# Kernel tuning notes

Hardware: AMD Instinct MI355X
Metric: run time of the kernel (lower is better)

## Reference

```python
import jax, jax.numpy as jnp
import numpy as np
from math import lgamma

# Architecture constants hardcoded in the original S2ConvNet
B_IN, B1, B2 = 30, 10, 6
F1, F2, F_OUT = 20, 40, 10
C64 = jnp.complex64


def _lf(n):
    return np.array([lgamma(i + 1.0) for i in range(n + 1)])


def _wigner_d(L, betas):
    """Padded Wigner-d tensor [L, nbeta, 2L-1, 2L-1]; entry [l,:,m+L-1,n+L-1] = d^l_{mn}(beta),
    zero where |m|>l or |n|>l. Explicit Wigner formula with log-factorials (stable for l<=30)."""
    nb = len(betas)
    out = np.zeros((L, nb, 2 * L - 1, 2 * L - 1))
    cb, sb = np.cos(betas / 2.0), np.sin(betas / 2.0)
    lf = _lf(4 * L)
    for l in range(L):
        for m in range(-l, l + 1):
            for n in range(-l, l + 1):
                pref = 0.5 * (lf[l + m] + lf[l - m] + lf[l + n] + lf[l - n])
                acc = np.zeros(nb)
                for s in range(max(0, n - m), min(l + n, l - m) + 1):
                    c = pref - (lf[l + n - s] + lf[s] + lf[m - n + s] + lf[l - m - s])
                    acc += (-1.0) ** (m - n + s) * np.exp(c) * cb ** (2 * l + n - m - 2 * s) * sb ** (m - n + 2 * s)
                out[l, :, m + L - 1, n + L - 1] = acc
    return out


def _dh_beta(b):
    return np.pi * (2 * np.arange(2 * b) + 1) / (4.0 * b)


def _dh_w(b):
    # Driscoll-Healy quadrature weights over the beta ring
    beta = _dh_beta(b)
    j = np.arange(b)
    return (2.0 / b) * np.sin(beta) * np.sum(np.sin((2 * j[:, None] + 1) * beta[None, :]) / (2 * j[:, None] + 1), axis=0)


def _s2_grid(max_beta=np.pi / 8, n_alpha=8, n_beta=3):
    beta = (np.arange(n_beta) + 1) * max_beta / n_beta
    alpha = np.linspace(0, 2 * np.pi, n_alpha, endpoint=False)
    B, A = np.meshgrid(beta, alpha, indexing='ij')
    return B.ravel(), A.ravel()


def _so3_grid(max_beta=np.pi / 8, n_alpha=8, n_beta=3, n_gamma=6):
    beta = (np.arange(n_beta) + 1) * max_beta / n_beta
    alpha = np.linspace(0, 2 * np.pi, n_alpha, endpoint=False)
    gamma = np.linspace(0, 2 * np.pi, n_gamma, endpoint=False)
    B, A, G = np.meshgrid(beta, alpha, gamma, indexing='ij')
    return B.ravel(), A.ravel(), G.ravel()


# ---- precomputed spectral constants (trace-time numpy) ----
_m1 = np.arange(-(B1 - 1), B1)            # 19 retained azimuthal freqs for b_l1
_m2 = np.arange(-(B2 - 1), B2)            # 11 retained freqs for b_l2
_mi_in = _m1 % (2 * B_IN)                 # wrap into fft bins of size 60
_mi_b1 = _m1 % (2 * B1)                   # wrap into bins of size 20
_mi2_b1 = _m2 % (2 * B1)
_mi2_b2 = _m2 % (2 * B2)

# S2 FFT: quadrature-weighted d^l_{m,0}(beta_k) on the b_in beta grid  [10,60,19]
_wd_s2 = (_dh_w(B_IN)[None, :, None] * _wigner_d(B1, _dh_beta(B_IN))[:, :, :, B1 - 1]).astype(np.float32)
# S2 kernel rft basis: conj spherical harmonics at the 24 near-identity grid pts  [10,24,19]
_bg, _ag = _s2_grid()
_Y1 = (_wigner_d(B1, _bg)[:, :, :, B1 - 1] * np.exp(-1j * _m1[None, :] * _ag[:, None])[None]).astype(np.complex64)
# SO3 inverse FFT synthesis matrices (incl. (2l+1) plancherel weight)  [10,20,19,19]
_d1w = (_wigner_d(B1, _dh_beta(B1)) * (2 * np.arange(B1) + 1)[:, None, None, None]).astype(np.float32)
# SO3 forward FFT analysis matrices (quadrature-weighted)  [6,20,11,11]
_d12w = (_wigner_d(B2, _dh_beta(B1)) * _dh_w(B1)[None, :, None, None]).astype(np.float32)
# SO3 kernel rft basis: conj Wigner-D at the 144 grid pts  [6,144,11,11]
_bg2, _ag2, _gg2 = _so3_grid()
_D2 = (_wigner_d(B2, _bg2) * np.exp(-1j * (_m2[None, :, None] * _ag2[:, None, None] + _m2[None, None, :] * _gg2[:, None, None]))[None]).astype(np.complex64)
_d2w = (_wigner_d(B2, _dh_beta(B2)) * (2 * np.arange(B2) + 1)[:, None, None, None]).astype(np.float32)
_w2n = (_dh_w(B2) / _dh_w(B2).sum()).astype(np.float32)


def _forward(x, psi1, psi2, w_lin, b_lin):
    B = x.shape[0]
    # ---- S2Convolution: azimuthal FFT + Legendre transform -> spectral outer product -> SO3 iFFT
    xf = jnp.fft.fft(x, axis=-1)[..., _mi_in]                       # [B,1,60,19] (beta, m)
    X = jnp.einsum('lbm,zcbm->lzcm', jnp.asarray(_wd_s2), xf)        # [10,B,1,19]
    Psi1 = jnp.einsum('iog,lgm->liom', psi1.astype(C64), jnp.asarray(_Y1))  # [10,1,20,19]
    F = jnp.einsum('lzcm,lcon->lzomn', X, Psi1)                      # [10,B,20,19,19]
    Fh = jnp.einsum('lzomn,lbmn->zobmn', F, jnp.asarray(_d1w))       # [B,20,20beta,19,19]
    full = jnp.zeros((B, F1, 2 * B1, 2 * B1, 2 * B1), C64).at[..., _mi_b1[:, None], _mi_b1[None, :]].set(Fh)
    y = jax.nn.relu(jnp.fft.ifft2(full, axes=(-2, -1)).real * (2 * B1) ** 2)  # [B,20,20,20,20] (beta,alpha,gamma)

    # ---- SO3Convolution: SO3 FFT -> per-l batched complex matmul -> SO3 iFFT
    yf = jnp.fft.fftn(y, axes=(-2, -1))[..., _mi2_b1[:, None], _mi2_b1[None, :]]  # [B,20,20,11,11]
    Fx = jnp.einsum('lbmn,zcbmn->lzcmn', jnp.asarray(_d12w), yf)     # [6,B,20,11,11]
    Psi2 = jnp.einsum('iog,lgmn->liomn', psi2.astype(C64), jnp.asarray(_D2))      # [6,20,40,11,11]
    Fo = jnp.einsum('lzimk,liokn->lzomn', Fx, Psi2)                  # [6,B,40,11,11]
    Fh2 = jnp.einsum('lzomn,lbmn->zobmn', Fo, jnp.asarray(_d2w))     # [B,40,12beta,11,11]
    full2 = jnp.zeros((B, F2, 2 * B2, 2 * B2, 2 * B2), C64).at[..., _mi2_b2[:, None], _mi2_b2[None, :]].set(Fh2)
    y2 = jax.nn.relu(jnp.fft.ifft2(full2, axes=(-2, -1)).real * (2 * B2) ** 2)    # [B,40,12,12,12]

    # ---- so3_integrate (beta quadrature, uniform alpha/gamma) + linear head
    feat = jnp.einsum('zobag,b->zo', y2, jnp.asarray(_w2n)) / (2 * B2) ** 2       # [B,40]
    return feat @ w_lin.T + b_lin


def setup_inputs() -> dict:
    key = jax.random.key(0)
    k1, k2, k3, k4, k5 = jax.random.split(key, 5)
    return {
        'x': jax.random.normal(k1, (128, 1, 60, 60), jnp.float32),
        'psi1': jax.random.normal(k2, (1, 20, 24), jnp.float32) * 0.1,
        'psi2': jax.random.normal(k3, (20, 40, 144), jnp.float32) * 0.05,
        'w_lin': jax.random.normal(k4, (10, 40), jnp.float32) * 0.1,
        'b_lin': jax.random.normal(k5, (10,), jnp.float32) * 0.1,
    }


def reference(x, psi1, psi2, w_lin, b_lin):
    return _forward(x, psi1, psi2, w_lin, b_lin)
```

## Files before the change

kernel.cpp:

```cpp
#include <hip/hip_runtime.h>
#include <math.h>

#define PI_D 3.14159265358979323846
#define PI_F 3.14159265358979f

#define BATCH 128
#define NM1 19
#define NMP1 10
#define NM2 11
#define NMP2 6
#define NB_IN 60
#define NB1 20
#define NB2 12
#define NL1 10
#define NL2 6
#define F1C 20
#define F2C 40
#define NBC 5

#define GEMM_MH (BATCH*NMP2)
#define GEMM_N (F2C*NM2)
#define GEMM_K (F1C*NM2)
#define GM 64
#define GN 64
#define GK 20
#define ASTR 21

#define TW_SYNT 0
#define TW_SYNA 380
#define TW_ANAA 580
#define TW_ANAG 700
#define TW_S2   940
#define TW_60   1072
#define TW_TOT  1672

#define TTS 22

#define N_D1WC 40000
#define N_D12WC 7920
#define N_WIGY 570
#define N_WIGD2 2178
#define N_D2W  (NL2*NB2*NM2*NM2)
#define N_WDS2C 6000
#define N_W2N  (NB2)
#define N_CSMALL (N_WIGY+N_WIGD2+N_WDS2C+N_W2N)
#define N_CPREP (N_D1WC+N_D12WC+N_D2W)
#define PREP_BASE (BATCH + 1 + 120)
#define NBLK_CPREP ((N_CPREP + 255)/256)

__device__ __forceinline__ float ipow_f(float x, int e) {
  float r = 1.f;
  for (int i = 0; i < e; ++i) r *= x;
  return r;
}

__device__ float wigdf(const float* lf, int l, int m, int n, float beta) {
  if (m < -l || m > l || n < -l || n > l) return 0.f;
  float cb = cosf(0.5f*beta), sb = sinf(0.5f*beta);
  float pref = 0.5f*(lf[l+m]+lf[l-m]+lf[l+n]+lf[l-n]);
  int s0 = (n-m) > 0 ? (n-m) : 0;
  int s1 = (l+n) < (l-m) ? (l+n) : (l-m);
  float acc = 0.f;
  for (int s = s0; s <= s1; ++s) {
    float lc = pref - (lf[l+n-s]+lf[s]+lf[m-n+s]+lf[l-m-s]);
    float tt = expf(lc) * ipow_f(cb, 2*l+n-m-2*s) * ipow_f(sb, m-n+2*s);
    acc += ((m-n+s) & 1) ? -tt : tt;
  }
  return acc;
}

__device__ __forceinline__ float dh_beta_f(int b, int k) {
  return (float)(PI_D*(2*k+1)/(4.0*b));
}

__device__ float dh_w_f(int b, int k) {
  float beta = dh_beta_f(b, k), s = 0.f;
  for (int j = 0; j < b; ++j) s += sinf((2.f*(float)j+1.f)*beta)/(2.f*(float)j+1.f);
  return (2.f/(float)b)*sinf(beta)*s;
}

__global__ __launch_bounds__(256) void k_consts1(float2* __restrict__ Tg,
                         float* __restrict__ wigY, float* __restrict__ wigD2,
                         float* __restrict__ wd_s2c, float* __restrict__ w2n) {
  __shared__ float lf[41];
  __shared__ float dhw30[60], dhw6[12];
  int t = threadIdx.x;
  if (t < 41) lf[t] = (float)lgamma((double)t + 1.0);
  else if (t < 101) dhw30[t-41] = dh_w_f(30, t-41);
  else if (t < 113) dhw6[t-101] = dh_w_f(6, t-101);
  __syncthreads();

  if (blockIdx.x == 0) {
    for (int i = t; i < TW_TOT; i += 256) {
      float2 v;
      if (i < TW_SYNA) {
        int j = i, n = j/NB1, g = j%NB1;
        int r = (g*(n-9)) % NB1; if (r < 0) r += NB1;
        float s, c; sincosf(2.f*PI_F*(float)r/(float)NB1, &s, &c);
        v = make_float2(c, s);
      } else if (i < TW_ANAA) {
        int j = i - TW_SYNA, a = j/NMP1, mp = j%NMP1;
        int r = (a*mp) % NB1;
        float s, c; sincosf(2.f*PI_F*(float)r/(float)NB1, &s, &c);
        v = make_float2(c, s);
      } else if (i < TW_ANAG) {
        int j = i - TW_ANAA, a = j/NMP2, m2p = j%NMP2;
        int r = (a*m2p) % NB1;
        float s, c; sincosf(2.f*PI_F*(float)r/(float)NB1, &s, &c);
        v = make_float2(c, -s);
      } else if (i < TW_S2) {
        int j = i - TW_ANAG, g = j/12, cI = j%12;
        if (cI == 11) v = make_float2(0.f, 0.f);
        else {
          int r = (g*(cI-5)) % NB1; if (r < 0) r += NB1;
          float s, c; sincosf(2.f*PI_F*(float)r/(float)NB1, &s, &c);
          v = make_float2(c, -s);
        }
      } else if (i < TW_60) {
        int j = i - TW_S2, k = j/NM2, mi = j%NM2;
        int r = (k*(mi-5)) % NB2; if (r < 0) r += NB2;
        float s, c; sincosf(2.f*PI_F*(float)r/(float)NB2, &s, &c);
        v = make_float2(c, s);
      } else {
        int j = i - TW_60, a = j/NMP1, mp = j%NMP1;
        int r = (a*mp) % NB_IN;
        float s, c; sincosf(2.f*PI_F*(float)r/(float)NB_IN, &s, &c);
        v = make_float2(c, -s);
      }
      Tg[i] = v;
    }
  }

  int gid = blockIdx.x*blockDim.x + t;

  if (gid < N_WIGY) {
    int l = gid/57; int r = gid%57; int bidx = r/19; int mi = r%19;
    float beta = (float)((double)(bidx + 1) * PI_D/24.0);
    wigY[gid] = wigdf(lf, l, mi-9, 0, beta);
    return;
  }
  gid -= N_WIGY;
  if (gid < N_WIGD2) {
    int l = gid/363; int r = gid%363; int bidx = r/121; int mn = r%121;
    int m = mn/NM2 - 5, n = mn%NM2 - 5;
    float beta = (float)((double)(bidx + 1) * PI_D/24.0);
    wigD2[gid] = wigdf(lf, l, m, n, beta);
    return;
  }
  gid -= N_WIGD2;
  if (gid < N_WDS2C) {
    int l = gid/600; int r = gid%600; int k = r/10; int mp = r%10;
    wd_s2c[gid] = dhw30[k] * wigdf(lf, l, mp, 0, dh_beta_f(30,k));
    return;
  }
  gid -= N_WDS2C;
  if (gid < N_W2N) {
    float s = 0.f;
    for (int j = 0; j < NB2; ++j) s += dhw6[j];
    w2n[gid] = dhw6[gid]/s;
    return;
  }
}

#define P2IO 40
#define P2GC 24
__global__ __launch_bounds__(256) void k_prep(const float* __restrict__ x,
                                              const float* __restrict__ wd_s2c,
                                              const float2* __restrict__ Tg,
                                              const float* __restrict__ wigY,
                                              const float* __restrict__ wigD2,
                                              const float* __restrict__ psi1,
                                              const float* __restrict__ psi2,
                                              float2* __restrict__ X,
                                              float2* __restrict__ Psi1p,
                                              float2* __restrict__ Bm,
                                              float* __restrict__ d1wc,
                                              float* __restrict__ d12wc,
                                              float* __restrict__ d2w) {
  __shared__ __align__(16) float smem[6912];
  const int bid = blockIdx.x, t = threadIdx.x;

  if (bid < BATCH) {
    const int z = bid;
    float*  xs   = smem;
    float2* xf   = (float2*)(smem + 3600);
    float2* tw60 = (float2*)(smem + 4800);
    for (int i = t; i < NB_IN*NMP1; i += 256) tw60[i] = Tg[TW_60 + i];
    for (int i = t; i < 3600; i += 256) xs[i] = x[z*3600 + i];
    __syncthreads();
    for (int i = t; i < NB_IN*NMP1; i += 256) {
      int k = i/NMP1, mp = i%NMP1;
      float re = 0.f, im = 0.f;
      const float* xrow = &xs[k*NB_IN];
      for (int a = 0; a < NB_IN; ++a) {
        float v = xrow[a];
        float2 e = tw60[a*NMP1 + mp];
        re = fmaf(v, e.x, re);
        im = fmaf(v, e.y, im);
      }
      xf[i] = make_float2(re, im);
    }
    __syncthreads();
    for (int i = t; i < NL1*NMP1; i += 256) {
      int l = i/NMP1, mp = i%NMP1;
      float re = 0.f, im = 0.f;
      for (int k = 0; k < NB_IN; ++k) {
        float w = wd_s2c[(l*NB_IN+k)*NMP1 + mp];
        float2 v = xf[k*NMP1 + mp];
        re = fmaf(w, v.x, re); im = fmaf(w, v.y, im);
      }
      X[(l*BATCH + z)*NMP1 + mp] = make_float2(re, im);
    }
    return;
  }

  if (bid == BATCH) {
    float*  wigYs = smem;
    float*  psis  = smem + 576;
    float2* ph8   = (float2*)(smem + 1056);
    for (int i = t; i < N_WIGY; i += 256) wigYs[i] = wigY[i];
    for (int i = t; i < F1C*24; i += 256) psis[i] = psi1[i];
    if (t < 8) {
      float s, c; sincosf(2.f*PI_F*(float)t/8.f, &s, &c);
      ph8[t] = make_float2(c, s);
    }
    __syncthreads();
    for (int i = t; i < NL1*F1C*NM1; i += 256) {
      int l = i/(F1C*NM1); int r = i%(F1C*NM1); int o = r/NM1; int mi = r%NM1;
      int m = mi - 9;
      float re = 0.f, im = 0.f;
      for (int g = 0; g < 24; ++g) {
        float w = psis[o*24 + g];
        float d = wigYs[(l*3 + (g >> 3))*NM1 + mi];
        int pa = g & 7;
        int rr = (-(m*pa)) % 8; if (rr < 0) rr += 8;
        float2 ph = ph8[rr];
        re = fmaf(w, d*ph.x, re); im = fmaf(w, d*ph.y, im);
      }
      Psi1p[i] = make_float2(re, im);
    }
    return;
  }

  if (bid < PREP_BASE) {
    const int j = bid - (BATCH + 1);
    const int io0 = (j/NL2)*P2IO, l = j%NL2;
    float2* Ds   = (float2*)smem;
    float*  Ws   = smem + 5856;
    float2* ph24 = (float2*)(smem + 6816);
    const int tio = t/31, tmn = t%31;
    const int mn0 = tmn*4;
    if (t < 24) {
      float s, c; sincosf(2.f*PI_F*(float)t/24.f, &s, &c);
      ph24[t] = make_float2(c, s);
    }
    __syncthreads();
    float2 acc[5][4];
    #pragma unroll
    for (int i = 0; i < 5; ++i)
      #pragma unroll
      for (int jj = 0; jj < 4; ++jj) acc[i][jj] = make_float2(0.f, 0.f);

    for (int gc = 0; gc < 144; gc += P2GC) {
      for (int i = t; i < P2GC*121; i += 256) {
        int g = i/121, mn = i%121;
        int p = gc + g;
        int m = mn/NM2 - 5, n = mn%NM2 - 5;
        float d = wigD2[(l*3 + p/48)*121 + mn];
        int pa = (p/6)%8, pg = p%6;
        int rr24 = (-(3*m*pa + 4*n*pg)) % 24; if (rr24 < 0) rr24 += 24;
        float2 ph = ph24[rr24];
        Ds[g*122 + mn] = make_float2(d*ph.x, d*ph.y);
      }
      for (int i = t; i < P2IO*P2GC; i += 256) {
        int io = i/P2GC, g = i%P2GC;
        Ws[i] = psi2[(io0 + io)*144 + gc + g];
      }
      __syncthreads();
      if (tio < 8) {
        for (int g = 0; g < P2GC; ++g) {
          float4 d01 = *(const float4*)&Ds[g*122 + mn0];
          float4 d23 = *(const float4*)&Ds[g*122 + mn0 + 2];
          float w0 = Ws[(tio*5 + 0)*P2GC + g];
          float w1 = Ws[(tio*5 + 1)*P2GC + g];
          float w2 = Ws[(tio*5 + 2)*P2GC + g];
          float w3 = Ws[(tio*5 + 3)*P2GC + g];
          float w4 = Ws[(tio*5 + 4)*P2GC + g];
          float dx[4] = {d01.x, d01.z, d23.x, d23.z};
          float dy[4] = {d01.y, d01.w, d23.y, d23.w};
          float wv[5] = {w0, w1, w2, w3, w4};
          #pragma unroll
          for (int i = 0; i < 5; ++i)
            #pragma unroll
            for (int jj = 0; jj < 4; ++jj) {
              acc[i][jj].x = fmaf(wv[i], dx[jj], acc[i][jj].x);
              acc[i][jj].y = fmaf(wv[i], dy[jj], acc[i][jj].y);
            }
        }
      }
      __syncthreads();
    }
    if (tio < 8) {
      #pragma unroll
      for (int i = 0; i < 5; ++i) {
        int io = io0 + tio*5 + i;
        int ii = io/F2C, oo = io%F2C;
        #pragma unroll
        for (int jj = 0; jj < 4; ++jj) {
          int mn = mn0 + jj;
          if (mn < 121) {
            int k = mn/NM2, n = mn%NM2;
            Bm[(size_t)l*GEMM_K*GEMM_N + (ii*NM2 + k)*GEMM_N + oo*NM2 + n] = acc[i][jj];
          }
        }
      }
    }
    return;
  }

  {
    float* lf     = smem;
    float* dhw10l = smem + 48;
    if (t < 41) lf[t] = (float)lgamma((double)t + 1.0);
    else if (t >= 64 && t < 84) dhw10l[t-64] = dh_w_f(10, t-64);
    __syncthreads();
    int idx = (bid - PREP_BASE)*256 + t;
    if (idx < N_D1WC) {
      int l = idx/4000; int r = idx%4000; int b = r/200; int r2 = r%200;
      int mp = r2/20, nn = r2%20;
      d1wc[idx] = (nn < NM1) ? (float)(2*l+1) * wigdf(lf, l, mp, nn-9, dh_beta_f(10,b)) : 0.f;
      return;
    }
    idx -= N_D1WC;
    if (idx < N_D12WC) {
      int l2 = idx/1320; int r = idx%1320; int b = r/66; int r2 = r%66;
      int m2p = r2/11, n2i = r2%11;
      d12wc[idx] = dhw10l[b] * wigdf(lf, l2, m2p, n2i-5, dh_beta_f(10,b));
      return;
    }
    idx -= N_D12WC;
    if (idx < N_D2W) {
      int l = idx/(NB2*NM2*NM2); int r = idx%(NB2*NM2*NM2); int j = r/(NM2*NM2); int rr = r%(NM2*NM2);
      int m = rr/NM2 - 5, n = rr%NM2 - 5;
      d2w[idx] = (float)(2*l+1) * wigdf(lf, l, m, n, dh_beta_f(6,j));
      return;
    }
  }
}

__global__ __launch_bounds__(256) void k_stage1(const float2* __restrict__ X,
                                                const float2* __restrict__ Psi1,
                                                const float* __restrict__ d1wc,
                                                const float* __restrict__ d12wc,
                                                const float2* __restrict__ Tg,
                                                float2* __restrict__ Am) {
  __shared__ float2 Xs[NL1*NMP1];
  __shared__ float2 Ps[NL1*NM1];
  __shared__ __align__(16) float2 XPp[NL1*NMP1*20];
  __shared__ __align__(16) float2 Etab[978];
  __shared__ __align__(16) float2 bufA[NBC*200];
  __shared__ __align__(16) float2 bufB[NBC*220];
  __shared__ float2 yfs[NBC*NMP2*NM2];
  __shared__ float2 Fxa[NL2*NMP2*NM2];

  const int z = blockIdx.x, o = blockIdx.y, t = threadIdx.x;
  const float2* EsynTp = Etab;
  const float2* EsynA  = Etab + 418;
  const float2* EanaA  = Etab + 618;
  const float2* EanaG  = Etab + 738;

  for (int i = t; i < 978; i += 256) {
    float2 v;
    if (i < 418) {
      int n = i/TTS, g = i%TTS;
      v = (g < NB1) ? Tg[TW_SYNT + n*NB1 + g] : make_float2(0.f, 0.f);
    } else {
      v = Tg[TW_SYNA + (i - 418)];
    }
    Etab[i] = v;
  }
  for (int i = t; i < NL1*NMP1; i += 256) {
    int l = i/NMP1, mp = i%NMP1;
    Xs[i] = X[(l*BATCH + z)*NMP1 + mp];
  }
  for (int i = t; i < NL1*NM1; i += 256) {
    int l = i/NM1, mi = i%NM1;
    Ps[i] = Psi1[(l*F1C + o)*NM1 + mi];
  }
  for (int i = t; i < NL2*NMP2*NM2; i += 256) Fxa[i] = make_float2(0.f, 0.f);
  __syncthreads();

  for (int i = t; i < NL1*NMP1*20; i += 256) {
    int n = i % 20; int r = i/20; int mp = r % NMP1; int l = r/NMP1;
    float2 v = make_float2(0.f, 0.f);
    if (n < NM1) {
      float2 xa = Xs[l*NMP1+mp], pp = Ps[l*NM1+n];
      v = make_float2(xa.x*pp.x - xa.y*pp.y, xa.x*pp.y + xa.y*pp.x);
    }
    XPp[i] = v;
  }
  __syncthreads();

  float2* Fh = bufA;
  float2* Tt = bufB;
  float*  yb = (float*)bufA;
  float2* Uu = bufB;

  for (int c = 0; c < NB1/NBC; ++c) {
    const int b0 = c*NBC;
    for (int i = t; i < NBC*NMP1*5; i += 256) {
      int q = i % 5; int r = i/5; int mp = r % NMP1; int bb = r/NMP1;
      int n0 = q*4;
      const float* dw = &d1wc[((b0+bb)*NMP1 + mp)*20 + n0];
      const float2* xp = &XPp[mp*20 + n0];
      float2 a0 = {0.f,0.f}, a1 = {0.f,0.f}, a2 = {0.f,0.f}, a3 = {0.f,0.f};
      #pragma unroll
      for (int l = 0; l < NL1; ++l) {
        float4 w4 = *(const float4*)&dw[l*4000];
        float4 xa = *(const float4*)&xp[l*(NMP1*20)];
        float4 xb = *(const float4*)&xp[l*(NMP1*20) + 2];
        a0.x = fmaf(w4.x, xa.x, a0.x); a0.y = fmaf(w4.x, xa.y, a0.y);
        a1.x = fmaf(w4.y, xa.z, a1.x); a1.y = fmaf(w4.y, xa.w, a1.y);
        a2.x = fmaf(w4.z, xb.x, a2.x); a2.y = fmaf(w4.z, xb.y, a2.y);
        a3.x = fmaf(w4.w, xb.z, a3.x); a3.y = fmaf(w4.w, xb.w, a3.y);
      }
      float2* fr = &Fh[(bb*NMP1 + mp)*NM1 + n0];
      fr[0] = a0; fr[1] = a1; fr[2] = a2;
      if (n0 + 3 < NM1) fr[3] = a3;
    }
    __syncthreads();
    for (int i = t; i < NBC*NMP1*5; i += 256) {
      int gq = i % 5; int r = i / 5; int mp = r % NMP1; int bb = r / NMP1;
      int g0 = gq*4;
      const float2* fh = &Fh[(bb*NMP1 + mp)*NM1];
      float2 a0 = {0.f,0.f}, a1 = {0.f,0.f}, a2 = {0.f,0.f}, a3 = {0.f,0.f};
      #pragma unroll
      for (int n = 0; n < NM1; ++n) {
        float2 f = fh[n];
        float4 e01 = *(const float4*)&EsynTp[n*TTS + g0];
        float4 e23 = *(const float4*)&EsynTp[n*TTS + g0 + 2];
        a0.x += f.x*e01.x - f.y*e01.y; a0.y += f.x*e01.y + f.y*e01.x;
        a1.x += f.x*e01.z - f.y*e01.w; a1.y += f.x*e01.w + f.y*e01.z;
        a2.x += f.x*e23.x - f.y*e23.y; a2.y += f.x*e23.y + f.y*e23.x;
        a3.x += f.x*e23.z - f.y*e23.w; a3.y += f.x*e23.w + f.y*e23.z;
      }
      float2* tr = &Tt[(bb*NMP1 + mp)*TTS + g0];
      tr[0] = a0; tr[1] = a1; tr[2] = a2; tr[3] = a3;
    }
    __syncthreads();
    for (int i = t; i < NBC*10*5; i += 256) {
      int gq = i % 5; int r = i / 5; int ap = r % 10; int bb = r / 10;
      int a0 = ap*2, g0 = gq*4;
      float4 t01 = *(const float4*)&Tt[(bb*NMP1)*TTS + g0];
      float4 t23 = *(const float4*)&Tt[(bb*NMP1)*TTS + g0 + 2];
      float s00=0.f,s01=0.f,s02=0.f,s03=0.f, s10=0.f,s11=0.f,s12=0.f,s13=0.f;
      #pragma unroll
      for (int mp = 1; mp < NMP1; ++mp) {
        float4 u01 = *(const float4*)&Tt[(bb*NMP1 + mp)*TTS + g0];
        float4 u23 = *(const float4*)&Tt[(bb*NMP1 + mp)*TTS + g0 + 2];
        float2 e0 = EsynA[a0*NMP1 + mp];
        float2 e1 = EsynA[(a0+1)*NMP1 + mp];
        s00 += e0.x*u01.x - e0.y*u01.y;
        s01 += e0.x*u01.z - e0.y*u01.w;
        s02 += e0.x*u23.x - e0.y*u23.y;
        s03 += e0.x*u23.z - e0.y*u23.w;
        s10 += e1.x*u01.x - e1.y*u01.y;
        s11 += e1.x*u01.z - e1.y*u01.w;
        s12 += e1.x*u23.x - e1.y*u23.y;
        s13 += e1.x*u23.z - e1.y*u23.w;
      }
      float* y0 = &yb[(bb*NB1 + a0)*NB1 + g0];
      float* y1 = &yb[(bb*NB1 + a0 + 1)*NB1 + g0];
      y0[0]=fmaxf(fmaf(2.f,s00,t01.x),0.f); y0[1]=fmaxf(fmaf(2.f,s01,t01.z),0.f);
      y0[2]=fmaxf(fmaf(2.f,s02,t23.x),0.f); y0[3]=fmaxf(fmaf(2.f,s03,t23.z),0.f);
      y1[0]=fmaxf(fmaf(2.f,s10,t01.x),0.f); y1[1]=fmaxf(fmaf(2.f,s11,t01.z),0.f);
      y1[2]=fmaxf(fmaf(2.f,s12,t23.x),0.f); y1[3]=fmaxf(fmaf(2.f,s13,t23.z),0.f);
    }
    __syncthreads();
    for (int i = t; i < NBC*NMP2*5; i += 256) {
      int gq = i % 5; int r = i / 5; int m2p = r % NMP2; int bb = r / NMP2;
      int g0 = gq*4;
      float2 u0 = {0.f,0.f}, u1 = {0.f,0.f}, u2 = {0.f,0.f}, u3 = {0.f,0.f};
      #pragma unroll
      for (int aa = 0; aa < NB1; ++aa) {
        float4 y4 = *(const float4*)&yb[(bb*NB1 + aa)*NB1 + g0];
        float2 e = EanaA[aa*NMP2 + m2p];
        u0.x = fmaf(y4.x, e.x, u0.x); u0.y = fmaf(y4.x, e.y, u0.y);
        u1.x = fmaf(y4.y, e.x, u1.x); u1.y = fmaf(y4.y, e.y, u1.y);
        u2.x = fmaf(y4.z, e.x, u2.x); u2.y = fmaf(y4.z, e.y, u2.y);
        u3.x = fmaf(y4.w, e.x, u3.x); u3.y = fmaf(y4.w, e.y, u3.y);
      }
      float2* ur = &Uu[(bb*NMP2 + m2p)*TTS + g0];
      ur[0] = u0; ur[1] = u1; ur[2] = u2; ur[3] = u3;
    }
    __syncthreads();
    for (int i = t; i < NBC*NMP2*6; i += 256) {
      int p = i % 6; int r = i / 6; int m2p = r % NMP2; int bb = r / NMP2;
      int n0 = p*2;
      const float2* ur = &Uu[(bb*NMP2 + m2p)*TTS];
      float2 acc0 = {0.f,0.f}, acc1 = {0.f,0.f};
      #pragma unroll
      for (int g = 0; g < NB1; ++g) {
        float2 u = ur[g];
        float4 e = *(const float4*)&EanaG[g*12 + n0];
        acc0.x += u.x*e.x - u.y*e.y; acc0.y += u.x*e.y + u.y*e.x;
        acc1.x += u.x*e.z - u.y*e.w; acc1.y += u.x*e.w + u.y*e.z;
      }
      yfs[(bb*NMP2 + m2p)*NM2 + n0] = acc0;
      if (n0 + 1 < NM2) yfs[(bb*NMP2 + m2p)*NM2 + n0 + 1] = acc1;
    }
    __syncthreads();
    for (int i = t; i < NL2*NMP2*NM2; i += 256) {
      int l2 = i/(NMP2*NM2); int r = i%(NMP2*NM2);
      float2 acc = Fxa[i];
      #pragma unroll
      for (int bb = 0; bb < NBC; ++bb) {
        float w = d12wc[(l2*NB1 + b0 + bb)*66 + r];
        float2 v = yfs[bb*(NMP2*NM2) + r];
        acc.x = fmaf(w, v.x, acc.x); acc.y = fmaf(w, v.y, acc.y);
      }
      Fxa[i] = acc;
    }
    __syncthreads();
  }
  for (int i = t; i < NL2*NMP2*NM2; i += 256) {
    int l2 = i/(NMP2*NM2); int r = i%(NMP2*NM2);
    int mp = r/NM2, n = r%NM2;
    Am[(size_t)l2*GEMM_MH*GEMM_K + (z*NMP2 + mp)*GEMM_K + o*NM2 + n] = Fxa[i];
  }
}

__global__ __launch_bounds__(256) void k_so3mm(const float2* __restrict__ A,
                                               const float2* __restrict__ B,
                                               float2* __restrict__ C0,
                                               float2* __restrict__ C1) {
  __shared__ float2 As[GM*ASTR];
  __shared__ float2 Bs[GK*GN];
  const int lz = blockIdx.z;
  const int l = lz >> 1, half = lz & 1;
  const int kbeg = half ? 120 : 0, klim = half ? 220 : 120;
  const int row0 = blockIdx.x*GM, col0 = blockIdx.y*GN;
  const int t = threadIdx.x;
  const float2* Ag = A + (size_t)l*GEMM_MH*GEMM_K;
  const float2* Bg = B + (size_t)l*GEMM_K*GEMM_N;
  float2* Cg = (half ? C1 : C0) + (size_t)l*GEMM_MH*GEMM_N;
  const int tn = t & 15, tm = t >> 4;
  float2 acc[4][4];
  #pragma unroll
  for (int i = 0; i < 4; ++i)
    #pragma unroll
    for (int j = 0; j < 4; ++j) acc[i][j] = make_float2(0.f, 0.f);

  for (int k0 = kbeg; k0 < klim; k0 += GK) {
    for (int i = t; i < GM*GK; i += 256) {
      int r = i/GK, kk = i%GK;
      As[r*ASTR + kk] = Ag[(size_t)(row0 + r)*GEMM_K + k0 + kk];
    }
    for (int i = t; i < GK*GN; i += 256) {
      int kk = i/GN, cc = i%GN;
      int col = col0 + cc;
      float2 v = (col < GEMM_N) ? Bg[(size_t)(k0 + kk)*GEMM_N + col] : make_float2(0.f, 0.f);
      Bs[(kk*4 + (cc & 3))*16 + (cc >> 2)] = v;
    }
    __syncthreads();
    #pragma unroll
    for (int kk = 0; kk < GK; ++kk) {
      float2 a[4], b[4];
      #pragma unroll
      for (int i = 0; i < 4; ++i) a[i] = As[(tm*4 + i)*ASTR + kk];
      #pragma unroll
      for (int j = 0; j < 4; ++j) b[j] = Bs[(kk*4 + j)*16 + tn];
      #pragma unroll
      for (int i = 0; i < 4; ++i)
        #pragma unroll
        for (int j = 0; j < 4; ++j) {
          acc[i][j].x = fmaf(a[i].x, b[j].x, acc[i][j].x);
          acc[i][j].x = fmaf(-a[i].y, b[j].y, acc[i][j].x);
          acc[i][j].y = fmaf(a[i].x, b[j].y, acc[i][j].y);
          acc[i][j].y = fmaf(a[i].y, b[j].x, acc[i][j].y);
        }
    }
    __syncthreads();
  }
  #pragma unroll
  for (int i = 0; i < 4; ++i) {
    int r = row0 + tm*4 + i;
    int c0 = col0 + tn*4;
    if (c0 < GEMM_N) {
      float4 v0 = make_float4(acc[i][0].x, acc[i][0].y, acc[i][1].x, acc[i][1].y);
      float4 v1 = make_float4(acc[i][2].x, acc[i][2].y, acc[i][3].x, acc[i][3].y);
      *(float4*)&Cg[(size_t)r*GEMM_N + c0] = v0;
      *(float4*)&Cg[(size_t)r*GEMM_N + c0 + 2] = v1;
    }
  }
}

__global__ __launch_bounds__(256) void k_stage2(const float2* __restrict__ C0,
                                                const float2* __restrict__ C1,
                                                const float* __restrict__ d2w,
                                                const float* __restrict__ w2n,
                                                const float2* __restrict__ Tg,
                                                float* __restrict__ feat) {
  __shared__ float2 Fos[NL2*NM2*NM2];
  __shared__ float2 Fh2[NB2*NM2*NM2];
  __shared__ float2 T2[NB2*NB2*NM2];
  __shared__ float2 Esyn2[NB2*NM2];
  __shared__ float w2s[NB2];
  __shared__ float wred[4];
  const int z = blockIdx.x, o = blockIdx.y, t = threadIdx.x;
  for (int i = t; i < NB2*NM2; i += 256) Esyn2[i] = Tg[TW_S2 + i];
  if (t < NB2) w2s[t] = w2n[t];
  for (int i = t; i < NL2*NM2*NM2; i += 256) {
    int l = i/(NM2*NM2); int mn = i%(NM2*NM2);
    int m = mn/NM2, n = mn%NM2;
    float2 v;
    if (m >= 5) {
      size_t idx = (size_t)l*GEMM_MH*GEMM_N + (size_t)(z*NMP2 + m - 5)*GEMM_N + o*NM2 + n;
      float2 a = C0[idx], b2 = C1[idx];
      v = make_float2(a.x + b2.x, a.y + b2.y);
    } else {
      size_t idx = (size_t)l*GEMM_MH*GEMM_N + (size_t)(z*NMP2 + 5 - m)*GEMM_N + o*NM2 + (10 - n);
      float2 a = C0[idx], b2 = C1[idx];
      float s = ((m - n) & 1) ? -1.f : 1.f;
      v = make_float2(s*(a.x + b2.x), -s*(a.y + b2.y));
    }
    Fos[i] = v;
  }
  __syncthreads();
  for (int i = t; i < NB2*NM2*NM2; i += 256) {
    int b = i/(NM2*NM2); int mn = i%(NM2*NM2);
    float re = 0.f, im = 0.f;
    #pragma unroll
    for (int l = 0; l < NL2; ++l) {
      float w = d2w[(l*NB2 + b)*(NM2*NM2) + mn];
      float2 v = Fos[l*(NM2*NM2) + mn];
      re = fmaf(w, v.x, re); im = fmaf(w, v.y, im);
    }
    Fh2[i] = make_float2(re, im);
  }
  __syncthreads();
  for (int i = t; i < NB2*NB2*NM2; i += 256) {
    int ni = i % NM2; int r = i / NM2; int aa = r % NB2; int b = r / NB2;
    const float2* fh = &Fh2[b*(NM2*NM2) + ni];
    float re = 0.f, im = 0.f;
    #pragma unroll
    for (int mi = 0; mi < NM2; ++mi) {
      float2 f = fh[mi*NM2]; float2 e = Esyn2[aa*NM2+mi];
      re += e.x*f.x - e.y*f.y;
      im += e.x*f.y + e.y*f.x;
    }
    T2[i] = make_float2(re, im);
  }
  __syncthreads();
  float accT = 0.f;
  for (int i = t; i < NB2*NB2*NB2; i += 256) {
    int g = i % NB2; int r = i / NB2; int aa = r % NB2; int b = r / NB2;
    const float2* trow = &T2[(b*NB2 + aa)*NM2];
    float v = 0.f;
    #pragma unroll
    for (int ni = 0; ni < NM2; ++ni) {
      float2 tv = trow[ni]; float2 e = Esyn2[g*NM2+ni];
      v += e.x*tv.x - e.y*tv.y;
    }
    accT += w2s[b]*fmaxf(v, 0.f);
  }
  #pragma unroll
  for (int off = 32; off > 0; off >>= 1) accT += __shfl_down(accT, off);
  if ((t & 63) == 0) wred[t >> 6] = accT;
  __syncthreads();
  if (t == 0) feat[z*F2C + o] = (wred[0]+wred[1]+wred[2]+wred[3]) / (float)(NB2*NB2);
}

__global__ void k_head(const float* __restrict__ feat, const float* __restrict__ w_lin,
                       const float* __restrict__ b_lin, float* __restrict__ out) {
  int idx = blockIdx.x*blockDim.x + threadIdx.x;
  if (idx >= BATCH*10) return;
  int z = idx/10, f = idx%10;
  float acc = b_lin[f];
  for (int o = 0; o < F2C; ++o) acc = fmaf(feat[z*F2C + o], w_lin[f*F2C + o], acc);
  out[idx] = acc;
}

extern "C" void kernel_launch(void* const* d_in, const int* in_sizes, int n_in,
                              void* d_out, int out_size, void* d_ws, size_t ws_size,
                              hipStream_t stream) {
  const float* x     = (const float*)d_in[0];
  const float* psi1  = (const float*)d_in[1];
  const float* psi2  = (const float*)d_in[2];
  const float* w_lin = (const float*)d_in[3];
  const float* b_lin = (const float*)d_in[4];
  float* out = (float*)d_out;
  float* ws  = (float*)d_ws;

  size_t off = 0;
  auto alloc = [&](size_t nfloats) { size_t o = off; off += (nfloats + 15) & ~(size_t)15; return o; };
  float2* Tglob = (float2*)(ws + alloc(2*TW_TOT));
  float*  d1wc  = ws + alloc(N_D1WC);
  float*  d12wc = ws + alloc(N_D12WC);
  float*  wigY  = ws + alloc(N_WIGY);
  float*  wigD2 = ws + alloc(N_WIGD2);
  float*  d2w   = ws + alloc(N_D2W);
  float*  wd_s2c= ws + alloc(N_WDS2C);
  float*  w2n   = ws + alloc(N_W2N);
  float2* X     = (float2*)(ws + alloc(2*(size_t)NL1*BATCH*NMP1));
  float2* Psi1p = (float2*)(ws + alloc(2*(size_t)NL1*F1C*NM1));
  float2* Bmat  = (float2*)(ws + alloc(2*(size_t)NL2*GEMM_K*GEMM_N));
  float2* Amat  = (float2*)(ws + alloc(2*(size_t)NL2*GEMM_MH*GEMM_K));
  float2* Cmat0 = (float2*)(ws + alloc(2*(size_t)NL2*GEMM_MH*GEMM_N));
  float2* Cmat1 = (float2*)(ws + alloc(2*(size_t)NL2*GEMM_MH*GEMM_N));
  float*  featp = ws + alloc((size_t)BATCH*F2C);
  if (ws_size < off*sizeof(float)) return;

  k_consts1<<<(N_CSMALL + 255)/256, 256, 0, stream>>>(Tglob, wigY, wigD2, wd_s2c, w2n);
  k_prep<<<PREP_BASE + NBLK_CPREP, 256, 0, stream>>>(x, wd_s2c, Tglob, wigY, wigD2,
                                                     psi1, psi2, X, Psi1p, Bmat,
                                                     d1wc, d12wc, d2w);
  k_stage1<<<dim3(BATCH, F1C), 256, 0, stream>>>(X, Psi1p, d1wc, d12wc, Tglob, Amat);
  k_so3mm<<<dim3(GEMM_MH/GM, (GEMM_N + GN - 1)/GN, 2*NL2), 256, 0, stream>>>(Amat, Bmat, Cmat0, Cmat1);
  k_stage2<<<dim3(BATCH, F2C), 256, 0, stream>>>(Cmat0, Cmat1, d2w, w2n, Tglob, featp);
  k_head<<<(BATCH*10 + 255)/256, 256, 0, stream>>>(featp, w_lin, b_lin, out);
}
```

Baseline: 284.4 us.

## Widen stage1 blocks to 512 threads and split GEMM K four ways

Stage1 now runs 512 threads per block and handles 10 beta rings per chunk instead of 5. Each phase becomes a single guarded pass, which halves the chunk iterations and the barriers. The padded twiddle table is replaced by a direct copy, and Ps/Xs now alias bufA. The SO(3) GEMM splits K into four partial products written to four buffers, which stage2 sums, giving the GEMM more blocks to schedule at the cost of extra partial-buffer traffic and more shared memory per stage1 block.

Result: slower. 317.0 us (+11.5%).

```diff
diff --git a/kernel.cpp b/kernel.cpp
--- a/kernel.cpp
+++ b/kernel.cpp
@@ -16,7 +16,7 @@
 #define NL2 6
 #define F1C 20
 #define F2C 40
-#define NBC 5
+#define NBC 10
 
 #define GEMM_MH (BATCH*NMP2)
 #define GEMM_N (F2C*NM2)
@@ -33,8 +33,6 @@
 #define TW_S2   940
 #define TW_60   1072
 #define TW_TOT  1672
-
-#define TTS 22
 
 #define N_D1WC 40000
 #define N_D12WC 7920
@@ -348,49 +346,40 @@
   }
 }
 
-__global__ __launch_bounds__(256) void k_stage1(const float2* __restrict__ X,
+__global__ __launch_bounds__(512) void k_stage1(const float2* __restrict__ X,
                                                 const float2* __restrict__ Psi1,
                                                 const float* __restrict__ d1wc,
                                                 const float* __restrict__ d12wc,
                                                 const float2* __restrict__ Tg,
                                                 float2* __restrict__ Am) {
-  __shared__ float2 Xs[NL1*NMP1];
-  __shared__ float2 Ps[NL1*NM1];
   __shared__ __align__(16) float2 XPp[NL1*NMP1*20];
-  __shared__ __align__(16) float2 Etab[978];
-  __shared__ __align__(16) float2 bufA[NBC*200];
-  __shared__ __align__(16) float2 bufB[NBC*220];
+  __shared__ __align__(16) float2 Etab[940];
+  __shared__ __align__(16) float2 bufA[2000];
+  __shared__ __align__(16) float2 bufB[2000];
   __shared__ float2 yfs[NBC*NMP2*NM2];
   __shared__ float2 Fxa[NL2*NMP2*NM2];
 
   const int z = blockIdx.x, o = blockIdx.y, t = threadIdx.x;
-  const float2* EsynTp = Etab;
-  const float2* EsynA  = Etab + 418;
-  const float2* EanaA  = Etab + 618;
-  const float2* EanaG  = Etab + 738;
-
-  for (int i = t; i < 978; i += 256) {
-    float2 v;
-    if (i < 418) {
-      int n = i/TTS, g = i%TTS;
-      v = (g < NB1) ? Tg[TW_SYNT + n*NB1 + g] : make_float2(0.f, 0.f);
-    } else {
-      v = Tg[TW_SYNA + (i - 418)];
-    }
-    Etab[i] = v;
-  }
-  for (int i = t; i < NL1*NMP1; i += 256) {
+  const float2* EsynT = Etab;
+  const float2* EsynA = Etab + 380;
+  const float2* EanaA = Etab + 580;
+  const float2* EanaG = Etab + 700;
+  float2* Ps = bufA;
+  float2* Xs = bufA + 190;
+
+  for (int i = t; i < 940; i += 512) Etab[i] = Tg[i];
+  for (int i = t; i < NL1*NMP1; i += 512) {
     int l = i/NMP1, mp = i%NMP1;
     Xs[i] = X[(l*BATCH + z)*NMP1 + mp];
   }
-  for (int i = t; i < NL1*NM1; i += 256) {
+  for (int i = t; i < NL1*NM1; i += 512) {
     int l = i/NM1, mi = i%NM1;
     Ps[i] = Psi1[(l*F1C + o)*NM1 + mi];
   }
-  for (int i = t; i < NL2*NMP2*NM2; i += 256) Fxa[i] = make_float2(0.f, 0.f);
+  for (int i = t; i < NL2*NMP2*NM2; i += 512) Fxa[i] = make_float2(0.f, 0.f);
   __syncthreads();
 
-  for (int i = t; i < NL1*NMP1*20; i += 256) {
+  for (int i = t; i < NL1*NMP1*20; i += 512) {
     int n = i % 20; int r = i/20; int mp = r % NMP1; int l = r/NMP1;
     float2 v = make_float2(0.f, 0.f);
     if (n < NM1) {
@@ -408,8 +397,8 @@
 
   for (int c = 0; c < NB1/NBC; ++c) {
     const int b0 = c*NBC;
-    for (int i = t; i < NBC*NMP1*5; i += 256) {
-      int q = i % 5; int r = i/5; int mp = r % NMP1; int bb = r/NMP1;
+    if (t < 500) {
+      int q = t % 5; int r = t/5; int mp = r % NMP1; int bb = r/NMP1;
       int n0 = q*4;
       const float* dw = &d1wc[((b0+bb)*NMP1 + mp)*20 + n0];
       const float2* xp = &XPp[mp*20 + n0];
@@ -429,35 +418,35 @@
       if (n0 + 3 < NM1) fr[3] = a3;
     }
     __syncthreads();
-    for (int i = t; i < NBC*NMP1*5; i += 256) {
-      int gq = i % 5; int r = i / 5; int mp = r % NMP1; int bb = r / NMP1;
+    if (t < 500) {
+      int gq = t % 5; int r = t / 5; int mp = r % NMP1; int bb = r / NMP1;
       int g0 = gq*4;
       const float2* fh = &Fh[(bb*NMP1 + mp)*NM1];
       float2 a0 = {0.f,0.f}, a1 = {0.f,0.f}, a2 = {0.f,0.f}, a3 = {0.f,0.f};
       #pragma unroll
       for (int n = 0; n < NM1; ++n) {
         float2 f = fh[n];
-        float4 e01 = *(const float4*)&EsynTp[n*TTS + g0];
-        float4 e23 = *(const float4*)&EsynTp[n*TTS + g0 + 2];
+        float4 e01 = *(const float4*)&EsynT[n*NB1 + g0];
+        float4 e23 = *(const float4*)&EsynT[n*NB1 + g0 + 2];
         a0.x += f.x*e01.x - f.y*e01.y; a0.y += f.x*e01.y + f.y*e01.x;
         a1.x += f.x*e01.z - f.y*e01.w; a1.y += f.x*e01.w + f.y*e01.z;
         a2.x += f.x*e23.x - f.y*e23.y; a2.y += f.x*e23.y + f.y*e23.x;
         a3.x += f.x*e23.z - f.y*e23.w; a3.y += f.x*e23.w + f.y*e23.z;
       }
-      float2* tr = &Tt[(bb*NMP1 + mp)*TTS + g0];
+      float2* tr = &Tt[(bb*NMP1 + mp)*NB1 + g0];
       tr[0] = a0; tr[1] = a1; tr[2] = a2; tr[3] = a3;
     }
     __syncthreads();
-    for (int i = t; i < NBC*10*5; i += 256) {
-      int gq = i % 5; int r = i / 5; int ap = r % 10; int bb = r / 10;
+    if (t < 500) {
+      int gq = t % 5; int r = t / 5; int ap = r % 10; int bb = r / 10;
       int a0 = ap*2, g0 = gq*4;
-      float4 t01 = *(const float4*)&Tt[(bb*NMP1)*TTS + g0];
-      float4 t23 = *(const float4*)&Tt[(bb*NMP1)*TTS + g0 + 2];
+      float4 t01 = *(const float4*)&Tt[(bb*NMP1)*NB1 + g0];
+      float4 t23 = *(const float4*)&Tt[(bb*NMP1)*NB1 + g0 + 2];
       float s00=0.f,s01=0.f,s02=0.f,s03=0.f, s10=0.f,s11=0.f,s12=0.f,s13=0.f;
       #pragma unroll
       for (int mp = 1; mp < NMP1; ++mp) {
-        float4 u01 = *(const float4*)&Tt[(bb*NMP1 + mp)*TTS + g0];
-        float4 u23 = *(const float4*)&Tt[(bb*NMP1 + mp)*TTS + g0 + 2];
+        float4 u01 = *(const float4*)&Tt[(bb*NMP1 + mp)*NB1 + g0];
+        float4 u23 = *(const float4*)&Tt[(bb*NMP1 + mp)*NB1 + g0 + 2];
         float2 e0 = EsynA[a0*NMP1 + mp];
         float2 e1 = EsynA[(a0+1)*NMP1 + mp];
         s00 += e0.x*u01.x - e0.y*u01.y;
@@ -477,8 +466,8 @@
       y1[2]=fmaxf(fmaf(2.f,s12,t23.x),0.f); y1[3]=fmaxf(fmaf(2.f,s13,t23.z),0.f);
     }
     __syncthreads();
-    for (int i = t; i < NBC*NMP2*5; i += 256) {
-      int gq = i % 5; int r = i / 5; int m2p = r % NMP2; int bb = r / NMP2;
+    if (t < 300) {
+      int gq = t % 5; int r = t / 5; int m2p = r % NMP2; int bb = r / NMP2;
       int g0 = gq*4;
       float2 u0 = {0.f,0.f}, u1 = {0.f,0.f}, u2 = {0.f,0.f}, u3 = {0.f,0.f};
       #pragma unroll
@@ -490,14 +479,14 @@
         u2.x = fmaf(y4.z, e.x, u2.x); u2.y = fmaf(y4.z, e.y, u2.y);
         u3.x = fmaf(y4.w, e.x, u3.x); u3.y = fmaf(y4.w, e.y, u3.y);
       }
-      float2* ur = &Uu[(bb*NMP2 + m2p)*TTS + g0];
+      float2* ur = &Uu[(bb*NMP2 + m2p)*NB1 + g0];
       ur[0] = u0; ur[1] = u1; ur[2] = u2; ur[3] = u3;
     }
     __syncthreads();
-    for (int i = t; i < NBC*NMP2*6; i += 256) {
-      int p = i % 6; int r = i / 6; int m2p = r % NMP2; int bb = r / NMP2;
+    if (t < 360) {
+      int p = t % 6; int r = t / 6; int m2p = r % NMP2; int bb = r / NMP2;
       int n0 = p*2;
-      const float2* ur = &Uu[(bb*NMP2 + m2p)*TTS];
+      const float2* ur = &Uu[(bb*NMP2 + m2p)*NB1];
       float2 acc0 = {0.f,0.f}, acc1 = {0.f,0.f};
       #pragma unroll
       for (int g = 0; g < NB1; ++g) {
@@ -510,20 +499,20 @@
       if (n0 + 1 < NM2) yfs[(bb*NMP2 + m2p)*NM2 + n0 + 1] = acc1;
     }
     __syncthreads();
-    for (int i = t; i < NL2*NMP2*NM2; i += 256) {
-      int l2 = i/(NMP2*NM2); int r = i%(NMP2*NM2);
-      float2 acc = Fxa[i];
+    if (t < NL2*NMP2*NM2) {
+      int l2 = t/(NMP2*NM2); int r = t%(NMP2*NM2);
+      float2 acc = Fxa[t];
       #pragma unroll
       for (int bb = 0; bb < NBC; ++bb) {
         float w = d12wc[(l2*NB1 + b0 + bb)*66 + r];
         float2 v = yfs[bb*(NMP2*NM2) + r];
         acc.x = fmaf(w, v.x, acc.x); acc.y = fmaf(w, v.y, acc.y);
       }
-      Fxa[i] = acc;
-    }
-    __syncthreads();
-  }
-  for (int i = t; i < NL2*NMP2*NM2; i += 256) {
+      Fxa[t] = acc;
+    }
+    __syncthreads();
+  }
+  for (int i = t; i < NL2*NMP2*NM2; i += 512) {
     int l2 = i/(NMP2*NM2); int r = i%(NMP2*NM2);
     int mp = r/NM2, n = r%NM2;
     Am[(size_t)l2*GEMM_MH*GEMM_K + (z*NMP2 + mp)*GEMM_K + o*NM2 + n] = Fxa[i];
@@ -533,17 +522,19 @@
 __global__ __launch_bounds__(256) void k_so3mm(const float2* __restrict__ A,
                                                const float2* __restrict__ B,
                                                float2* __restrict__ C0,
-                                               float2* __restrict__ C1) {
+                                               float2* __restrict__ C1,
+                                               float2* __restrict__ C2,
+                                               float2* __restrict__ C3) {
   __shared__ float2 As[GM*ASTR];
   __shared__ float2 Bs[GK*GN];
   const int lz = blockIdx.z;
-  const int l = lz >> 1, half = lz & 1;
-  const int kbeg = half ? 120 : 0, klim = half ? 220 : 120;
+  const int l = lz >> 2, q = lz & 3;
+  const int kbeg = q*60, klim = (q == 3) ? 220 : (kbeg + 60);
   const int row0 = blockIdx.x*GM, col0 = blockIdx.y*GN;
   const int t = threadIdx.x;
   const float2* Ag = A + (size_t)l*GEMM_MH*GEMM_K;
   const float2* Bg = B + (size_t)l*GEMM_K*GEMM_N;
-  float2* Cg = (half ? C1 : C0) + (size_t)l*GEMM_MH*GEMM_N;
+  float2* Cg = (q == 0 ? C0 : (q == 1 ? C1 : (q == 2 ? C2 : C3))) + (size_t)l*GEMM_MH*GEMM_N;
   const int tn = t & 15, tm = t >> 4;
   float2 acc[4][4];
   #pragma unroll
@@ -597,6 +588,8 @@
 
 __global__ __launch_bounds__(256) void k_stage2(const float2* __restrict__ C0,
                                                 const float2* __restrict__ C1,
+                                                const float2* __restrict__ C2,
+                                                const float2* __restrict__ C3,
                                                 const float* __restrict__ d2w,
                                                 const float* __restrict__ w2n,
                                                 const float2* __restrict__ Tg,
@@ -613,18 +606,19 @@
   for (int i = t; i < NL2*NM2*NM2; i += 256) {
     int l = i/(NM2*NM2); int mn = i%(NM2*NM2);
     int m = mn/NM2, n = mn%NM2;
-    float2 v;
-    if (m >= 5) {
-      size_t idx = (size_t)l*GEMM_MH*GEMM_N + (size_t)(z*NMP2 + m - 5)*GEMM_N + o*NM2 + n;
-      float2 a = C0[idx], b2 = C1[idx];
-      v = make_float2(a.x + b2.x, a.y + b2.y);
+    size_t idx;
+    float sgn = 1.f;
+    bool mirror = (m < 5);
+    if (!mirror) {
+      idx = (size_t)l*GEMM_MH*GEMM_N + (size_t)(z*NMP2 + m - 5)*GEMM_N + o*NM2 + n;
     } else {
-      size_t idx = (size_t)l*GEMM_MH*GEMM_N + (size_t)(z*NMP2 + 5 - m)*GEMM_N + o*NM2 + (10 - n);
-      float2 a = C0[idx], b2 = C1[idx];
-      float s = ((m - n) & 1) ? -1.f : 1.f;
-      v = make_float2(s*(a.x + b2.x), -s*(a.y + b2.y));
-    }
-    Fos[i] = v;
+      idx = (size_t)l*GEMM_MH*GEMM_N + (size_t)(z*NMP2 + 5 - m)*GEMM_N + o*NM2 + (10 - n);
+      sgn = ((m - n) & 1) ? -1.f : 1.f;
+    }
+    float2 a = C0[idx], b2 = C1[idx], c2 = C2[idx], d2 = C3[idx];
+    float re = a.x + b2.x + c2.x + d2.x;
+    float im = a.y + b2.y + c2.y + d2.y;
+    Fos[i] = mirror ? make_float2(sgn*re, -sgn*im) : make_float2(re, im);
   }
   __syncthreads();
   for (int i = t; i < NB2*NM2*NM2; i += 256) {
@@ -708,6 +702,8 @@
   float2* Amat  = (float2*)(ws + alloc(2*(size_t)NL2*GEMM_MH*GEMM_K));
   float2* Cmat0 = (float2*)(ws + alloc(2*(size_t)NL2*GEMM_MH*GEMM_N));
   float2* Cmat1 = (float2*)(ws + alloc(2*(size_t)NL2*GEMM_MH*GEMM_N));
+  float2* Cmat2 = (float2*)(ws + alloc(2*(size_t)NL2*GEMM_MH*GEMM_N));
+  float2* Cmat3 = (float2*)(ws + alloc(2*(size_t)NL2*GEMM_MH*GEMM_N));
   float*  featp = ws + alloc((size_t)BATCH*F2C);
   if (ws_size < off*sizeof(float)) return;
 
@@ -715,8 +711,10 @@
   k_prep<<<PREP_BASE + NBLK_CPREP, 256, 0, stream>>>(x, wd_s2c, Tglob, wigY, wigD2,
                                                      psi1, psi2, X, Psi1p, Bmat,
                                                      d1wc, d12wc, d2w);
-  k_stage1<<<dim3(BATCH, F1C), 256, 0, stream>>>(X, Psi1p, d1wc, d12wc, Tglob, Amat);
-  k_so3mm<<<dim3(GEMM_MH/GM, (GEMM_N + GN - 1)/GN, 2*NL2), 256, 0, stream>>>(Amat, Bmat, Cmat0, Cmat1);
-  k_stage2<<<dim3(BATCH, F2C), 256, 0, stream>>>(Cmat0, Cmat1, d2w, w2n, Tglob, featp);
+  k_stage1<<<dim3(BATCH, F1C), 512, 0, stream>>>(X, Psi1p, d1wc, d12wc, Tglob, Amat);
+  k_so3mm<<<dim3(GEMM_MH/GM, (GEMM_N + GN - 1)/GN, 4*NL2), 256, 0, stream>>>(Amat, Bmat,
+                                                                             Cmat0, Cmat1, Cmat2, Cmat3);
+  k_stage2<<<dim3(BATCH, F2C), 256, 0, stream>>>(Cmat0, Cmat1, Cmat2, Cmat3,
+                                                 d2w, w2n, Tglob, featp);
   k_head<<<(BATCH*10 + 255)/256, 256, 0, stream>>>(featp, w_lin, b_lin, out);
 }
```
